# Performance work log

Hardware: AMD Instinct MI355X
Metric: run time of the kernel (lower is better)

Reference implementation:

```python
import jax, jax.numpy as jnp
import numpy as np

RES = 0.03
NUM_ROTS = 36
NUM_PROPOSAL = 256
OVERSAMPLE = 4           # fixed-size stand-in for the data-dependent while loop
GX, GY, GZ = 272, 112, 272  # grid covering [-4,4.16] x [-0.2,3.16] x [-4,4.16] at res=0.03
POW = 0.5
SEED_DIST_THRESH = 0.3


def setup_inputs() -> dict:
    key = jax.random.key(0)
    ks = jax.random.split(key, 6)
    N, M = 100000, 1024
    extent = jnp.array([7.0, 3.0, 7.0], jnp.float32)
    offset = jnp.array([-3.5, 0.0, -3.5], jnp.float32)
    pc = jax.random.uniform(ks[0], (N, 3), jnp.float32) * extent + offset
    xyz = jax.random.uniform(ks[1], (N, 3), jnp.float32, minval=-0.3, maxval=0.3)
    scale = jax.random.uniform(ks[2], (N, 3), jnp.float32, minval=0.1, maxval=1.0)
    prob = jax.random.uniform(ks[3], (N,), jnp.float32)
    corners = jnp.array([[-4.0, -0.2, -4.0], [4.16, 3.16, 4.16]], jnp.float32)
    vote_points = jax.random.uniform(ks[4], (M, 3), jnp.float32) * extent + offset
    return dict(pc=pc, xyz=xyz, scale=scale, prob=prob, corners=corners, vote_points=vote_points)


def hough_vote(pc, xyz, scale, prob, corners):
    # Each point casts NUM_ROTS votes: center = pc + R_y(theta) @ xyz_offset
    thetas = 2.0 * jnp.pi * jnp.arange(NUM_ROTS, dtype=jnp.float32) / NUM_ROTS
    c, s = jnp.cos(thetas), jnp.sin(thetas)  # [R]
    ox, oy, oz = xyz[:, 0:1], xyz[:, 1:2], xyz[:, 2:3]  # [N,1]
    rx = ox * c + oz * s      # [N,R]
    rz = -ox * s + oz * c     # [N,R]
    tx = pc[:, 0:1] + rx
    ty = jnp.broadcast_to(pc[:, 1:2] + oy, tx.shape)
    tz = pc[:, 2:3] + rz
    ix = jnp.floor((tx - corners[0, 0]) / RES + 0.5).astype(jnp.int32)
    iy = jnp.floor((ty - corners[0, 1]) / RES + 0.5).astype(jnp.int32)
    iz = jnp.floor((tz - corners[0, 2]) / RES + 0.5).astype(jnp.int32)
    inb = ((ix >= 0) & (ix < GX) & (iy >= 0) & (iy < GY) & (iz >= 0) & (iz < GZ))
    ixc = jnp.clip(ix, 0, GX - 1)
    iyc = jnp.clip(iy, 0, GY - 1)
    izc = jnp.clip(iz, 0, GZ - 1)
    flat = ((ixc * GY + iyc) * GZ + izc).ravel()  # [N*R]
    w = (prob[:, None] * inb.astype(prob.dtype))  # [N,R]
    grid_obj = jnp.zeros((GX * GY * GZ,), pc.dtype).at[flat].add(w.ravel())
    ws = (w[:, :, None] * scale[:, None, :]).reshape(-1, 3)
    grid_scale = jnp.zeros((GX * GY * GZ, 3), pc.dtype).at[flat].add(ws)
    hv_map = grid_obj.reshape(GX, GY, GZ)
    hv_scale = (grid_scale / (grid_obj[:, None] + 1e-7)).reshape(GX, GY, GZ, 3)
    return hv_map, hv_scale


def reference(pc, xyz, scale, prob, corners, vote_points):
    hv_map, hv_scale = hough_vote(pc, xyz, scale, prob, corners)
    hv_map_y = jnp.power(hv_map.max(axis=1) + 1e-7, POW)  # [GX,GZ]
    hv_map_yidx = jnp.argmax(hv_map, axis=1)              # [GX,GZ]
    dist = hv_map_y.reshape(-1)
    finite = jnp.isfinite(dist)
    safe = jnp.where(finite, dist, 0.0)
    ok = finite.all() & (safe.sum() >= 1e-7)
    dist = jnp.where(ok, safe, 1.0)

    # fixed-size oversampling instead of the data-dependent while loop
    K = NUM_PROPOSAL * OVERSAMPLE
    sample = jax.random.categorical(jax.random.key(42), jnp.log(dist + 1e-30), shape=(K,))
    sample_val = dist[sample]
    xi = sample // GZ
    zi = sample % GZ
    yi = hv_map_yidx[xi, zi]
    world_loc = jnp.stack([xi, yi, zi], -1).astype(pc.dtype) * RES + corners[0]  # [K,3]
    sc = hv_scale[xi, yi, zi, :]  # [K,3]

    # min distance to vote seeds; keep candidates near seeds (fallback: keep all)
    d2seed = jnp.min(jnp.linalg.norm(world_loc[:, None, :] - vote_points[None, :, :], axis=-1), axis=-1)
    keep = d2seed < SEED_DIST_THRESH
    keep = jnp.where(keep.any(), keep, jnp.ones_like(keep))
    order = jnp.argsort(jnp.where(keep, 0, 1))  # stable: passing candidates first
    sel = order[:NUM_PROPOSAL]
    candidates = world_loc[sel]
    scales_out = sc[sel]
    probs = jnp.zeros((NUM_PROPOSAL,), pc.dtype)
    return candidates, probs, scales_out
```

## Files before the change

### kernel.cpp

```cpp
#include <hip/hip_runtime.h>
#include <math.h>
#include <stdio.h>
#include <stdint.h>

#define GXD 272
#define GYD 112
#define GZD 272
#define NROT 36
#define CCLS (GXD*GZD)
#define KSMP 1024
#define NPROP 256
#define HSLOTS 2048
#define YH 56
#define NBINS (GXD*2)
#define SLICE (GYD*GZD)
#define SVCAP 64
#define ROWG 16

struct RotTab { float c[NROT]; float s[NROT]; };

__device__ __forceinline__ uint32_t cell_hash(int flat) {
    return ((uint32_t)flat * 2654435761u) >> 21;
}

#define ROTL_AB(x, r) __builtin_amdgcn_alignbit((x), (x), 32u - (r))

__device__ __forceinline__ void threefry2x32(uint32_t k0, uint32_t k1,
                                             uint32_t x0, uint32_t x1,
                                             uint32_t& o0, uint32_t& o1) {
    uint32_t ks2 = k0 ^ k1 ^ 0x1BD11BDAu;
#define TF_ROUND(r) { x0 += x1; x1 = ROTL_AB(x1, r); x1 ^= x0; }
    x0 += k0; x1 += k1;
    TF_ROUND(13) TF_ROUND(15) TF_ROUND(26) TF_ROUND(6)
    x0 += k1;  x1 += ks2 + 1u;
    TF_ROUND(17) TF_ROUND(29) TF_ROUND(16) TF_ROUND(24)
    x0 += ks2; x1 += k0 + 2u;
    TF_ROUND(13) TF_ROUND(15) TF_ROUND(26) TF_ROUND(6)
    x0 += k0;  x1 += k1 + 3u;
    TF_ROUND(17) TF_ROUND(29) TF_ROUND(16) TF_ROUND(24)
    x0 += k1;  x1 += ks2 + 4u;
    TF_ROUND(13) TF_ROUND(15) TF_ROUND(26) TF_ROUND(6)
    x0 += ks2; x1 += k0 + 5u;
#undef TF_ROUND
    o0 = x0; o1 = x1;
}

__device__ __forceinline__ uint32_t tf_bits(uint32_t i) {
    uint32_t o0, o1;
    threefry2x32(0u, 42u, 0u, i, o0, o1);
    return o0 ^ o1;
}

template<int W>
__device__ __forceinline__ void tf_batch(uint32_t ib, uint32_t* out) {
    constexpr uint32_t K1  = 42u;
    constexpr uint32_t KS2 = 0u ^ 42u ^ 0x1BD11BDAu;
    uint32_t x0[W], x1[W];
#pragma unroll
    for (int j = 0; j < W; ++j) {
        x0[j] = 0u;
        x1[j] = ib + (uint32_t)(j * CCLS) + K1;
    }
    constexpr uint32_t R[5][4]  = {{13,15,26,6},{17,29,16,24},{13,15,26,6},
                                   {17,29,16,24},{13,15,26,6}};
    constexpr uint32_t I0[5] = {K1, KS2, 0u, K1, KS2};
    constexpr uint32_t I1[5] = {KS2 + 1u, 2u, K1 + 3u, KS2 + 4u, 5u};
#pragma unroll
    for (int g = 0; g < 5; ++g) {
#pragma unroll
        for (int r = 0; r < 4; ++r) {
#pragma unroll
            for (int j = 0; j < W; ++j) {
                x0[j] += x1[j];
                x1[j] = ROTL_AB(x1[j], R[g][r]);
                x1[j] ^= x0[j];
            }
        }
#pragma unroll
        for (int j = 0; j < W; ++j) { x0[j] += I0[g]; x1[j] += I1[g]; }
    }
#pragma unroll
    for (int j = 0; j < W; ++j) out[j] = x0[j] ^ x1[j];
}

__device__ __forceinline__ float uniform_from_bits(uint32_t b) {
    const float TINY = 1.1754943508222875e-38f;
    float f = __uint_as_float((b >> 9) | 0x3f800000u) - 1.0f;
    float u = __fadd_rn(__fmul_rn(f, 1.0f), TINY);
    return fmaxf(TINY, u);
}

__device__ __forceinline__ float gumbel_from_u(float u) {
    float l1 = (float)log((double)u);
    float l2 = (float)log((double)(-l1));
    return -l2;
}

__device__ __forceinline__ bool vote_iy(float py, float oy, float c0y, int& iy) {
    float ty = __fadd_rn(py, oy);
    float vy = __fadd_rn(__fdiv_rn(__fsub_rn(ty, c0y), 0.03f), 0.5f);
    iy = (int)floorf(vy);
    return (iy >= 0 && iy < GYD);
}
__device__ __forceinline__ bool vote_xz(float px, float pz, float ox, float oz,
                                        float c, float s, float c0x, float c0z,
                                        int& ix, int& iz) {
    float rx = __fadd_rn(__fmul_rn(ox, c), __fmul_rn(oz, s));
    float rz = __fadd_rn(__fmul_rn(-ox, s), __fmul_rn(oz, c));
    float tx = __fadd_rn(px, rx);
    float tz = __fadd_rn(pz, rz);
    float vx = __fadd_rn(__fdiv_rn(__fsub_rn(tx, c0x), 0.03f), 0.5f);
    float vz = __fadd_rn(__fdiv_rn(__fsub_rn(tz, c0z), 0.03f), 0.5f);
    ix = (int)floorf(vx);
    iz = (int)floorf(vz);
    return (ix >= 0 && ix < GXD && iz >= 0 && iz < GZD);
}
__device__ __forceinline__ bool vote_cell(float px, float py, float pz,
                                          float ox, float oy, float oz,
                                          float c, float s,
                                          float c0x, float c0y, float c0z,
                                          int& flat) {
    int iy, ix, iz;
    if (!vote_iy(py, oy, c0y, iy)) return false;
    if (!vote_xz(px, pz, ox, oz, c, s, c0x, c0z, ix, iz)) return false;
    flat = (ix*GYD + iy)*GZD + iz;
    return true;
}

__global__ __launch_bounds__(256) void k_count(const float* __restrict__ pc, const float* __restrict__ xyz,
                          const float* __restrict__ corners, int N, RotTab rt,
                          int* __restrict__ bincnt) {
    __shared__ int h[NBINS];
    int tid = threadIdx.x;
    for (int j = tid; j < NBINS; j += 256) h[j] = 0;
    __syncthreads();
    int i = blockIdx.x * 256 + tid;
    if (i < N) {
        float px = pc[3*i], py = pc[3*i+1], pz = pc[3*i+2];
        float ox = xyz[3*i], oy = xyz[3*i+1], oz = xyz[3*i+2];
        int iy;
        if (vote_iy(py, oy, corners[1], iy)) {
            int ybit = (iy >= YH) ? 1 : 0;
            float c0x = corners[0], c0z = corners[2];
            for (int r = 0; r < NROT; ++r) {
                int ix, iz;
                if (vote_xz(px, pz, ox, oz, rt.c[r], rt.s[r], c0x, c0z, ix, iz))
                    atomicAdd(&h[ix*2 + ybit], 1);
            }
        }
    }
    __syncthreads();
    for (int j = tid; j < NBINS; j += 256) if (h[j]) atomicAdd(&bincnt[j], h[j]);
}

__global__ __launch_bounds__(576) void k_prefix(const int* __restrict__ bincnt,
                         int* __restrict__ binbase, int* __restrict__ bincur) {
    __shared__ int sc[576];
    int tid = threadIdx.x;
    int v = (tid < NBINS) ? bincnt[tid] : 0;
    sc[tid] = v;
    __syncthreads();
    for (int off = 1; off < 576; off <<= 1) {
        int x = sc[tid];
        if (tid >= off) x += sc[tid - off];
        __syncthreads();
        sc[tid] = x;
        __syncthreads();
    }
    if (tid < NBINS) {
        int excl = sc[tid] - v;
        binbase[tid] = excl;
        bincur[tid] = excl;
    }
}

__global__ __launch_bounds__(256) void k_binwrite(const float* __restrict__ pc, const float* __restrict__ xyz,
                          const float* __restrict__ prob, const float* __restrict__ corners,
                          int N, RotTab rt, int* __restrict__ bincur,
                          int* __restrict__ vflat, float* __restrict__ vw) {
    __shared__ int h[NBINS];
    __shared__ int bbase[NBINS];
    int tid = threadIdx.x;
    for (int j = tid; j < NBINS; j += 256) h[j] = 0;
    __syncthreads();
    int i = blockIdx.x * 256 + tid;
    float px=0, py=0, pz=0, ox=0, oy=0, oz=0, w0=0, c0x=0, c0z=0;
    int iy = -1, ybit = 0;
    bool act = false;
    if (i < N) {
        px = pc[3*i]; py = pc[3*i+1]; pz = pc[3*i+2];
        ox = xyz[3*i]; oy = xyz[3*i+1]; oz = xyz[3*i+2];
        w0 = prob[i];
        c0x = corners[0]; c0z = corners[2];
        if (vote_iy(py, oy, corners[1], iy)) {
            act = true;
            ybit = (iy >= YH) ? 1 : 0;
        }
    }
    if (act) {
        for (int r = 0; r < NROT; ++r) {
            int ix, iz;
            if (vote_xz(px, pz, ox, oz, rt.c[r], rt.s[r], c0x, c0z, ix, iz))
                atomicAdd(&h[ix*2 + ybit], 1);
        }
    }
    __syncthreads();
    for (int j = tid; j < NBINS; j += 256) {
        int cnt = h[j];
        bbase[j] = cnt ? atomicAdd(&bincur[j], cnt) : 0;
        h[j] = 0;
    }
    __syncthreads();
    if (act) {
        for (int r = 0; r < NROT; ++r) {
            int ix, iz;
            if (vote_xz(px, pz, ox, oz, rt.c[r], rt.s[r], c0x, c0z, ix, iz)) {
                int bin = ix*2 + ybit;
                int rank = atomicAdd(&h[bin], 1);
                int slot = bbase[bin] + rank;
                vflat[slot] = (ix*GYD + iy)*GZD + iz;
                vw[slot] = w0;
            }
        }
    }
}

__global__ __launch_bounds__(256) void k_accum(const int* __restrict__ binbase,
                          const int* __restrict__ bincnt,
                          const int* __restrict__ vflat, const float* __restrict__ vw,
                          float* __restrict__ gobj) {
    __shared__ float tile[YH*GZD];
    int b = blockIdx.x;
    int x = b >> 1, yh = b & 1;
    int tid = threadIdx.x;
    for (int j = tid; j < YH*GZD; j += 256) tile[j] = 0.0f;
    __syncthreads();
    int lo = binbase[b], n = bincnt[b];
    int xoff = x * SLICE;
    int yoff = yh * (YH*GZD);
    for (int j = lo + tid; j < lo + n; j += 256) {
        int rel = vflat[j] - xoff;
        atomicAdd(&tile[rel - yoff], vw[j]);
    }
    __syncthreads();
    float* dst = gobj + (size_t)xoff + yoff;
    for (int j = tid; j < YH*GZD; j += 256) dst[j] = tile[j];
}

__global__ __launch_bounds__(256) void k_colmax(const float* __restrict__ gobj,
                         float* __restrict__ logits, int* __restrict__ yidx,
                         float* __restrict__ sumdist) {
    int c = blockIdx.x * blockDim.x + threadIdx.x;
    float d = 0.0f;
    if (c < CCLS) {
        int x = c / GZD, z = c % GZD;
        const float* base = gobj + (size_t)x*GYD*GZD + z;
        float m = base[0];
        int mi = 0;
        for (int y = 1; y < GYD; ++y) {
            float v = base[(size_t)y*GZD];
            if (v > m) { m = v; mi = y; }
        }
        d = __fsqrt_rn(__fadd_rn(m, 1e-7f));
        yidx[c] = mi;
        logits[c] = (float)log((double)__fadd_rn(d, 1e-30f));
    }
    __shared__ float sred[256];
    int tid = threadIdx.x;
    sred[tid] = d; __syncthreads();
    for (int off = 128; off > 0; off >>= 1) {
        if (tid < off) sred[tid] += sred[tid+off];
        __syncthreads();
    }
    if (tid == 0) atomicAdd(sumdist, sred[0]);
}

__global__ __launch_bounds__(256) void k_thresh(const float* __restrict__ logits,
                                                const float* __restrict__ sumdist,
                                                uint32_t* __restrict__ bth) {
    int c = blockIdx.x * blockDim.x + threadIdx.x;
    if (c >= CCLS) return;
    double B0 = log((double)*sumdist) - 3.0;
    double t = exp(-exp((double)logits[c] - (B0 - 0.05)));
    long long k_th = (long long)floor(t * 8388608.0) - 2;
    uint32_t b;
    if (k_th <= 0)              b = 0u;
    else if (k_th >= 8388608LL) b = 0xFFFFFFFFu;
    else                        b = (uint32_t)k_th << 9;
    bth[c] = b;
}

__global__ __launch_bounds__(256) void k_prefilter(const uint32_t* __restrict__ bth,
                                                   int* __restrict__ svcnt,
                                                   uint2* __restrict__ svrec) {
    int c = blockIdx.x * 256 + threadIdx.x;
    int k0 = blockIdx.y * (KSMP / ROWG);
    uint32_t th = bth[c];
    uint32_t i = (uint32_t)k0 * (uint32_t)CCLS + (uint32_t)c;
#pragma unroll 1
    for (int kk = 0; kk < KSMP / ROWG; kk += 8) {
        uint32_t b[8];
        tf_batch<8>(i, b);
#pragma unroll
        for (int j = 0; j < 8; ++j) {
            if (__builtin_expect(b[j] >= th, 0)) {
                int row = k0 + kk + j;
                int idx = atomicAdd(&svcnt[row], 1);
                if (idx < SVCAP) svrec[row * SVCAP + idx] = make_uint2((uint32_t)c, b[j]);
            }
        }
        i += 8u * (uint32_t)CCLS;
    }
}

__global__ __launch_bounds__(256) void k_finalize(const float* __restrict__ logits,
                                                  const int* __restrict__ svcnt,
                                                  const uint2* __restrict__ svrec,
                                                  int* __restrict__ samples) {
    int k = blockIdx.x;
    int tid = threadIdx.x;
    int n = svcnt[k];
    float best = -INFINITY; int bc = 0x7fffffff;
    if (n > 0 && n <= SVCAP) {
        if (tid < n) {
            uint2 rec = svrec[k * SVCAP + tid];
            int c = (int)rec.x;
            best = __fadd_rn(gumbel_from_u(uniform_from_bits(rec.y)), logits[c]);
            bc = c;
        }
    } else {
        uint32_t base = (uint32_t)k * (uint32_t)CCLS;
        for (int c = tid; c < CCLS; c += 256) {
            float v = __fadd_rn(gumbel_from_u(uniform_from_bits(tf_bits(base + (uint32_t)c))), logits[c]);
            if (v > best || (v == best && c < bc)) { best = v; bc = c; }
        }
    }
    __shared__ float sv[256];
    __shared__ int   si[256];
    sv[tid] = best; si[tid] = bc; __syncthreads();
    for (int off = 128; off > 0; off >>= 1) {
        if (tid < off) {
            float v2 = sv[tid+off]; int i2 = si[tid+off];
            if (v2 > sv[tid] || (v2 == sv[tid] && i2 < si[tid])) { sv[tid] = v2; si[tid] = i2; }
        }
        __syncthreads();
    }
    if (tid == 0) samples[k] = si[0];
}

__global__ __launch_bounds__(256) void k_build_table(const int* __restrict__ samples,
                                                     const int* __restrict__ yidx,
                                                     int* __restrict__ hkeys,
                                                     float* __restrict__ gsmall) {
    int tid = threadIdx.x;
    for (int j = tid; j < HSLOTS; j += 256) hkeys[j] = -1;
    for (int j = tid; j < 3*HSLOTS; j += 256) gsmall[j] = 0.0f;
    __syncthreads();
    for (int k = tid; k < KSMP; k += 256) {
        int s = samples[k];
        int xi = s / GZD, zi = s % GZD;
        int yi = yidx[s];
        int flat = (xi*GYD + yi)*GZD + zi;
        uint32_t h = cell_hash(flat);
        for (;;) {
            int prev = atomicCAS(&hkeys[h], -1, flat);
            if (prev == -1 || prev == flat) break;
            h = (h + 1) & (HSLOTS - 1);
        }
    }
}

__global__ __launch_bounds__(256) void k_scale_scatter(const float* __restrict__ pc, const float* __restrict__ xyz,
                          const float* __restrict__ scale, const float* __restrict__ prob,
                          const float* __restrict__ corners,
                          const int* __restrict__ hkeys, float* __restrict__ gsmall,
                          int N, RotTab rt) {
    __shared__ int lk[HSLOTS];
    for (int j = threadIdx.x; j < HSLOTS; j += 256) lk[j] = hkeys[j];
    __syncthreads();
    int i = blockIdx.x * blockDim.x + threadIdx.x;
    int r = blockIdx.y;
    if (i >= N) return;
    int flat;
    if (!vote_cell(pc[3*i], pc[3*i+1], pc[3*i+2], xyz[3*i], xyz[3*i+1], xyz[3*i+2],
                   rt.c[r], rt.s[r], corners[0], corners[1], corners[2], flat)) return;
    uint32_t h = cell_hash(flat);
    int slot = -1;
    for (;;) {
        int key = lk[h];
        if (key == flat) { slot = (int)h; break; }
        if (key == -1) break;
        h = (h + 1) & (HSLOTS - 1);
    }
    if (slot < 0) return;
    float w0 = prob[i];
    atomicAdd(&gsmall[3*slot+0], __fmul_rn(w0, scale[3*i]));
    atomicAdd(&gsmall[3*slot+1], __fmul_rn(w0, scale[3*i+1]));
    atomicAdd(&gsmall[3*slot+2], __fmul_rn(w0, scale[3*i+2]));
}

__global__ __launch_bounds__(256) void k_post(const float* __restrict__ gobj,
                       const int* __restrict__ hkeys, const float* __restrict__ gsmall,
                       const int* __restrict__ yidx, const int* __restrict__ samples,
                       const float* __restrict__ corners, const float* __restrict__ vp, int M,
                       float* __restrict__ world, float* __restrict__ scv, int* __restrict__ keep) {
    int k = blockIdx.x;
    int tid = threadIdx.x;
    int s = samples[k];
    int xi = s / GZD, zi = s % GZD;
    int yi = yidx[s];
    float wx = __fadd_rn(__fmul_rn((float)xi, 0.03f), corners[0]);
    float wy = __fadd_rn(__fmul_rn((float)yi, 0.03f), corners[1]);
    float wz = __fadd_rn(__fmul_rn((float)zi, 0.03f), corners[2]);

    float dmin = INFINITY;
    for (int j = tid; j < M; j += 256) {
        float dx = __fsub_rn(wx, vp[3*j]);
        float dy = __fsub_rn(wy, vp[3*j+1]);
        float dz = __fsub_rn(wz, vp[3*j+2]);
        float sq = __fadd_rn(__fadd_rn(__fmul_rn(dx,dx), __fmul_rn(dy,dy)), __fmul_rn(dz,dz));
        dmin = fminf(dmin, __fsqrt_rn(sq));
    }
    __shared__ float sm[256];
    sm[tid] = dmin; __syncthreads();
    for (int off = 128; off > 0; off >>= 1) {
        if (tid < off) sm[tid] = fminf(sm[tid], sm[tid+off]);
        __syncthreads();
    }
    if (tid == 0) {
        world[3*k] = wx; world[3*k+1] = wy; world[3*k+2] = wz;
        int flat = (xi*GYD + yi)*GZD + zi;
        uint32_t h = cell_hash(flat);
        while (hkeys[h] != flat) h = (h + 1) & (HSLOTS - 1);
        float go = __fadd_rn(gobj[flat], 1e-7f);
        scv[3*k+0] = __fdiv_rn(gsmall[3*h+0], go);
        scv[3*k+1] = __fdiv_rn(gsmall[3*h+1], go);
        scv[3*k+2] = __fdiv_rn(gsmall[3*h+2], go);
        keep[k] = (sm[0] < 0.3f) ? 1 : 0;
    }
}

__global__ __launch_bounds__(256) void k_select(const float* __restrict__ world,
                                                const float* __restrict__ scv,
                                                const int* __restrict__ keep,
                                                float* __restrict__ out) {
    __shared__ int kp[KSMP];
    __shared__ int tsum[256];
    __shared__ int sel[NPROP];
    __shared__ int anyk;
    int tid = threadIdx.x;
    if (tid == 0) anyk = 0;
    __syncthreads();
    int a = 0;
    for (int j = tid; j < KSMP; j += 256) { int v = keep[j]; kp[j] = v; a |= v; }
    if (a) anyk = 1;
    __syncthreads();
    int any = anyk;
    int j0 = tid * 4;
    int k0v = any ? kp[j0]   : 1;
    int k1v = any ? kp[j0+1] : 1;
    int k2v = any ? kp[j0+2] : 1;
    int k3v = any ? kp[j0+3] : 1;
    int s0 = k0v, s1 = s0 + k1v, s2 = s1 + k2v, s3 = s2 + k3v;
    tsum[tid] = s3;
    __syncthreads();
    for (int off = 1; off < 256; off <<= 1) {
        int x = tsum[tid];
        if (tid >= off) x += tsum[tid - off];
        __syncthreads();
        tsum[tid] = x;
        __syncthreads();
    }
    int base = (tid > 0) ? tsum[tid-1] : 0;
    int nk = tsum[255];
    int inc[4] = { base + s0, base + s1, base + s2, base + s3 };
    int kv[4]  = { k0v, k1v, k2v, k3v };
    for (int q = 0; q < 4; ++q) {
        int j = j0 + q;
        int slot = kv[q] ? (inc[q] - 1) : (nk + j - inc[q]);
        if (slot < NPROP) sel[slot] = j;
    }
    __syncthreads();
    if (tid < NPROP) {
        int sidx = sel[tid];
        out[3*tid+0] = world[3*sidx+0];
        out[3*tid+1] = world[3*sidx+1];
        out[3*tid+2] = world[3*sidx+2];
        out[3*NPROP + tid] = 0.0f;
        out[4*NPROP + 3*tid + 0] = scv[3*sidx+0];
        out[4*NPROP + 3*tid + 1] = scv[3*sidx+1];
        out[4*NPROP + 3*tid + 2] = scv[3*sidx+2];
    }
}

extern "C" void kernel_launch(void* const* d_in, const int* in_sizes, int n_in,
                              void* d_out, int out_size, void* d_ws, size_t ws_size,
                              hipStream_t stream) {
    const float* pc      = (const float*)d_in[0];
    const float* xyz     = (const float*)d_in[1];
    const float* scale   = (const float*)d_in[2];
    const float* prob    = (const float*)d_in[3];
    const float* corners = (const float*)d_in[4];
    const float* vp      = (const float*)d_in[5];
    int N = in_sizes[0] / 3;
    int M = in_sizes[5] / 3;
    int NV = N * NROT;

    const size_t G = (size_t)GXD * GYD * GZD;
    float* gobj    = (float*)d_ws;
    float* sumdist = gobj + G;
    int*   bincnt  = (int*)(sumdist + 1);
    int*   svcnt   = bincnt + NBINS;
    int*   binbase = svcnt + KSMP;
    int*   bincur  = binbase + NBINS;
    float* logits  = (float*)(bincur + NBINS);
    uint32_t* bth  = (uint32_t*)(logits + CCLS);
    int*   yidx    = (int*)(bth + CCLS);
    int*   samples = yidx + CCLS;
    int*   hkeys   = samples + KSMP;
    float* gsmall  = (float*)(hkeys + HSLOTS);
    float* world   = gsmall + 3*HSLOTS;
    float* scv     = world + 3*KSMP;
    int*   keep    = (int*)(scv + 3*KSMP);
    uint2* svrec   = (uint2*)(((uintptr_t)(keep + KSMP) + 15) & ~(uintptr_t)15);
    int*   vflat   = (int*)(svrec + (size_t)KSMP * SVCAP);
    float* vw      = (float*)(vflat + NV);
    size_t need = (size_t)((char*)(vw + NV) - (char*)d_ws);
    if (ws_size < need) {
        fprintf(stderr, "kernel_launch: ws_size %zu < needed %zu\n", ws_size, need);
        return;
    }

    hipMemsetAsync(sumdist, 0, (1 + NBINS + KSMP)*sizeof(int), stream);

    RotTab rt;
    const float twopi = (float)(2.0 * M_PI);
    for (int r = 0; r < NROT; ++r) {
        float th = (twopi * (float)r) / 36.0f;
        rt.c[r] = (float)cos((double)th);
        rt.s[r] = (float)sin((double)th);
    }

    int pblocks = (N + 255) / 256;
    k_count<<<pblocks, 256, 0, stream>>>(pc, xyz, corners, N, rt, bincnt);
    k_prefix<<<1, 576, 0, stream>>>(bincnt, binbase, bincur);
    k_binwrite<<<pblocks, 256, 0, stream>>>(pc, xyz, prob, corners, N, rt, bincur, vflat, vw);
    k_accum<<<NBINS, 256, 0, stream>>>(binbase, bincnt, vflat, vw, gobj);
    k_colmax<<<(CCLS + 255) / 256, 256, 0, stream>>>(gobj, logits, yidx, sumdist);
    k_thresh<<<(CCLS + 255) / 256, 256, 0, stream>>>(logits, sumdist, bth);
    dim3 pf_grid(CCLS / 256, ROWG);
    k_prefilter<<<pf_grid, 256, 0, stream>>>(bth, svcnt, svrec);
    k_finalize<<<KSMP, 256, 0, stream>>>(logits, svcnt, svrec, samples);
    k_build_table<<<1, 256, 0, stream>>>(samples, yidx, hkeys, gsmall);
    dim3 sgrid(pblocks, NROT);
    k_scale_scatter<<<sgrid, 256, 0, stream>>>(pc, xyz, scale, prob, corners, hkeys, gsmall, N, rt);
    k_post<<<KSMP, 256, 0, stream>>>(gobj, hkeys, gsmall, yidx, samples, corners, vp, M, world, scv, keep);
    k_select<<<1, 256, 0, stream>>>(world, scv, keep, (float*)d_out);
}
```

Before: 420.7 us.

## Fuse column max into accumulation, interleave vote records, and restructure sampling kernels

Vote records are written as interleaved (flat, weight) pairs, and each accumulation block computes per-column partial maxima over its half-slice from shared memory. This removes the strided full-grid column scan, which now only merges two partials. The prefilter is split into two launches using different rotate instruction sequences, finalize drops to one wavefront with shuffle reduction, and scale scatter loops over rotations per thread instead of using a 2D grid. Together these trade some extra workspace and code complexity for less global traffic and fewer launches' worth of redundant per-point work.

```diff
diff --git a/kernel.cpp b/kernel.cpp
--- a/kernel.cpp
+++ b/kernel.cpp
@@ -24,6 +24,20 @@
 }
 
 #define ROTL_AB(x, r) __builtin_amdgcn_alignbit((x), (x), 32u - (r))
+
+template<int MODE, uint32_t R>
+__device__ __forceinline__ uint32_t rotl1(uint32_t x) {
+    if constexpr (MODE == 0) {
+        return ROTL_AB(x, R);
+    } else {
+        uint32_t t, d;
+        asm("v_lshrrev_b32 %0, %3, %2\n\t"
+            "v_lshl_or_b32 %1, %2, %4, %0"
+            : "=&v"(t), "=v"(d)
+            : "v"(x), "i"(32u - R), "i"(R));
+        return d;
+    }
+}
 
 __device__ __forceinline__ void threefry2x32(uint32_t k0, uint32_t k1,
                                              uint32_t x0, uint32_t x1,
@@ -51,7 +65,7 @@
     return o0 ^ o1;
 }
 
-template<int W>
+template<int W, int MODE>
 __device__ __forceinline__ void tf_batch(uint32_t ib, uint32_t* out) {
     constexpr uint32_t K1  = 42u;
     constexpr uint32_t KS2 = 0u ^ 42u ^ 0x1BD11BDAu;
@@ -61,24 +75,17 @@
         x0[j] = 0u;
         x1[j] = ib + (uint32_t)(j * CCLS) + K1;
     }
-    constexpr uint32_t R[5][4]  = {{13,15,26,6},{17,29,16,24},{13,15,26,6},
-                                   {17,29,16,24},{13,15,26,6}};
-    constexpr uint32_t I0[5] = {K1, KS2, 0u, K1, KS2};
-    constexpr uint32_t I1[5] = {KS2 + 1u, 2u, K1 + 3u, KS2 + 4u, 5u};
-#pragma unroll
-    for (int g = 0; g < 5; ++g) {
-#pragma unroll
-        for (int r = 0; r < 4; ++r) {
-#pragma unroll
-            for (int j = 0; j < W; ++j) {
-                x0[j] += x1[j];
-                x1[j] = ROTL_AB(x1[j], R[g][r]);
-                x1[j] ^= x0[j];
-            }
-        }
-#pragma unroll
-        for (int j = 0; j < W; ++j) { x0[j] += I0[g]; x1[j] += I1[g]; }
-    }
+#define TFB_ROUND(RR) _Pragma("unroll") \
+    for (int j = 0; j < W; ++j) { x0[j] += x1[j]; x1[j] = rotl1<MODE, RR>(x1[j]); x1[j] ^= x0[j]; }
+#define TFB_INJ(IA, IB) _Pragma("unroll") \
+    for (int j = 0; j < W; ++j) { x0[j] += (IA); x1[j] += (IB); }
+    TFB_ROUND(13) TFB_ROUND(15) TFB_ROUND(26) TFB_ROUND(6)  TFB_INJ(K1,  KS2 + 1u)
+    TFB_ROUND(17) TFB_ROUND(29) TFB_ROUND(16) TFB_ROUND(24) TFB_INJ(KS2, 2u)
+    TFB_ROUND(13) TFB_ROUND(15) TFB_ROUND(26) TFB_ROUND(6)  TFB_INJ(0u,  K1 + 3u)
+    TFB_ROUND(17) TFB_ROUND(29) TFB_ROUND(16) TFB_ROUND(24) TFB_INJ(K1,  KS2 + 4u)
+    TFB_ROUND(13) TFB_ROUND(15) TFB_ROUND(26) TFB_ROUND(6)  TFB_INJ(KS2, 5u)
+#undef TFB_ROUND
+#undef TFB_INJ
 #pragma unroll
     for (int j = 0; j < W; ++j) out[j] = x0[j] ^ x1[j];
 }
@@ -114,17 +121,6 @@
     ix = (int)floorf(vx);
     iz = (int)floorf(vz);
     return (ix >= 0 && ix < GXD && iz >= 0 && iz < GZD);
-}
-__device__ __forceinline__ bool vote_cell(float px, float py, float pz,
-                                          float ox, float oy, float oz,
-                                          float c, float s,
-                                          float c0x, float c0y, float c0z,
-                                          int& flat) {
-    int iy, ix, iz;
-    if (!vote_iy(py, oy, c0y, iy)) return false;
-    if (!vote_xz(px, pz, ox, oz, c, s, c0x, c0z, ix, iz)) return false;
-    flat = (ix*GYD + iy)*GZD + iz;
-    return true;
 }
 
 __global__ __launch_bounds__(256) void k_count(const float* __restrict__ pc, const float* __restrict__ xyz,
@@ -177,7 +173,7 @@
 __global__ __launch_bounds__(256) void k_binwrite(const float* __restrict__ pc, const float* __restrict__ xyz,
                           const float* __restrict__ prob, const float* __restrict__ corners,
                           int N, RotTab rt, int* __restrict__ bincur,
-                          int* __restrict__ vflat, float* __restrict__ vw) {
+                          uint2* __restrict__ vrec) {
     __shared__ int h[NBINS];
     __shared__ int bbase[NBINS];
     int tid = threadIdx.x;
@@ -218,8 +214,7 @@
                 int bin = ix*2 + ybit;
                 int rank = atomicAdd(&h[bin], 1);
                 int slot = bbase[bin] + rank;
-                vflat[slot] = (ix*GYD + iy)*GZD + iz;
-                vw[slot] = w0;
+                vrec[slot] = make_uint2((uint32_t)((ix*GYD + iy)*GZD + iz), __float_as_uint(w0));
             }
         }
     }
@@ -227,8 +222,9 @@
 
 __global__ __launch_bounds__(256) void k_accum(const int* __restrict__ binbase,
                           const int* __restrict__ bincnt,
-                          const int* __restrict__ vflat, const float* __restrict__ vw,
-                          float* __restrict__ gobj) {
+                          const uint2* __restrict__ vrec,
+                          float* __restrict__ gobj,
+                          float* __restrict__ cmax, int* __restrict__ camax) {
     __shared__ float tile[YH*GZD];
     int b = blockIdx.x;
     int x = b >> 1, yh = b & 1;
@@ -238,29 +234,40 @@
     int lo = binbase[b], n = bincnt[b];
     int xoff = x * SLICE;
     int yoff = yh * (YH*GZD);
+    int sub = xoff + yoff;
     for (int j = lo + tid; j < lo + n; j += 256) {
-        int rel = vflat[j] - xoff;
-        atomicAdd(&tile[rel - yoff], vw[j]);
-    }
-    __syncthreads();
-    float* dst = gobj + (size_t)xoff + yoff;
+        uint2 rec = vrec[j];
+        atomicAdd(&tile[(int)rec.x - sub], __uint_as_float(rec.y));
+    }
+    __syncthreads();
+    float* dst = gobj + (size_t)sub;
     for (int j = tid; j < YH*GZD; j += 256) dst[j] = tile[j];
-}
-
-__global__ __launch_bounds__(256) void k_colmax(const float* __restrict__ gobj,
+    for (int z = tid; z < GZD; z += 256) {
+        float m = tile[z];
+        int mi = 0;
+        for (int y = 1; y < YH; ++y) {
+            float v = tile[y*GZD + z];
+            if (v > m) { m = v; mi = y; }
+        }
+        cmax[b*GZD + z] = m;
+        camax[b*GZD + z] = mi;
+    }
+}
+
+__global__ __launch_bounds__(256) void k_colmax2(const float* __restrict__ cmax,
+                         const int* __restrict__ camax,
                          float* __restrict__ logits, int* __restrict__ yidx,
                          float* __restrict__ sumdist) {
     int c = blockIdx.x * blockDim.x + threadIdx.x;
     float d = 0.0f;
     if (c < CCLS) {
         int x = c / GZD, z = c % GZD;
-        const float* base = gobj + (size_t)x*GYD*GZD + z;
-        float m = base[0];
-        int mi = 0;
-        for (int y = 1; y < GYD; ++y) {
-            float v = base[(size_t)y*GZD];
-            if (v > m) { m = v; mi = y; }
-        }
+        int b0 = (x*2)*GZD + z;
+        int b1 = b0 + GZD;
+        float m0 = cmax[b0], m1 = cmax[b1];
+        float m; int mi;
+        if (m1 > m0) { m = m1; mi = YH + camax[b1]; }
+        else         { m = m0; mi = camax[b0]; }
         d = __fsqrt_rn(__fadd_rn(m, 1e-7f));
         yidx[c] = mi;
         logits[c] = (float)log((double)__fadd_rn(d, 1e-30f));
@@ -290,17 +297,19 @@
     bth[c] = b;
 }
 
-__global__ __launch_bounds__(256) void k_prefilter(const uint32_t* __restrict__ bth,
-                                                   int* __restrict__ svcnt,
-                                                   uint2* __restrict__ svrec) {
+template<int MODE>
+__global__ __launch_bounds__(256) void k_prefilter_t(const uint32_t* __restrict__ bth,
+                                                     int* __restrict__ svcnt,
+                                                     uint2* __restrict__ svrec,
+                                                     int kbase) {
     int c = blockIdx.x * 256 + threadIdx.x;
-    int k0 = blockIdx.y * (KSMP / ROWG);
+    int k0 = kbase + blockIdx.y * (KSMP / ROWG);
     uint32_t th = bth[c];
     uint32_t i = (uint32_t)k0 * (uint32_t)CCLS + (uint32_t)c;
 #pragma unroll 1
     for (int kk = 0; kk < KSMP / ROWG; kk += 8) {
         uint32_t b[8];
-        tf_batch<8>(i, b);
+        tf_batch<8, MODE>(i, b);
 #pragma unroll
         for (int j = 0; j < 8; ++j) {
             if (__builtin_expect(b[j] >= th, 0)) {
@@ -313,10 +322,10 @@
     }
 }
 
-__global__ __launch_bounds__(256) void k_finalize(const float* __restrict__ logits,
-                                                  const int* __restrict__ svcnt,
-                                                  const uint2* __restrict__ svrec,
-                                                  int* __restrict__ samples) {
+__global__ __launch_bounds__(64) void k_finalize(const float* __restrict__ logits,
+                                                 const int* __restrict__ svcnt,
+                                                 const uint2* __restrict__ svrec,
+                                                 int* __restrict__ samples) {
     int k = blockIdx.x;
     int tid = threadIdx.x;
     int n = svcnt[k];
@@ -330,22 +339,17 @@
         }
     } else {
         uint32_t base = (uint32_t)k * (uint32_t)CCLS;
-        for (int c = tid; c < CCLS; c += 256) {
+        for (int c = tid; c < CCLS; c += 64) {
             float v = __fadd_rn(gumbel_from_u(uniform_from_bits(tf_bits(base + (uint32_t)c))), logits[c]);
             if (v > best || (v == best && c < bc)) { best = v; bc = c; }
         }
     }
-    __shared__ float sv[256];
-    __shared__ int   si[256];
-    sv[tid] = best; si[tid] = bc; __syncthreads();
-    for (int off = 128; off > 0; off >>= 1) {
-        if (tid < off) {
-            float v2 = sv[tid+off]; int i2 = si[tid+off];
-            if (v2 > sv[tid] || (v2 == sv[tid] && i2 < si[tid])) { sv[tid] = v2; si[tid] = i2; }
-        }
-        __syncthreads();
-    }
-    if (tid == 0) samples[k] = si[0];
+    for (int off = 32; off > 0; off >>= 1) {
+        float v2 = __shfl_down(best, off);
+        int   i2 = __shfl_down(bc, off);
+        if (v2 > best || (v2 == best && i2 < bc)) { best = v2; bc = i2; }
+    }
+    if (tid == 0) samples[k] = bc;
 }
 
 __global__ __launch_bounds__(256) void k_build_table(const int* __restrict__ samples,
@@ -378,25 +382,35 @@
     __shared__ int lk[HSLOTS];
     for (int j = threadIdx.x; j < HSLOTS; j += 256) lk[j] = hkeys[j];
     __syncthreads();
-    int i = blockIdx.x * blockDim.x + threadIdx.x;
-    int r = blockIdx.y;
+    int i = blockIdx.x * 256 + threadIdx.x;
     if (i >= N) return;
-    int flat;
-    if (!vote_cell(pc[3*i], pc[3*i+1], pc[3*i+2], xyz[3*i], xyz[3*i+1], xyz[3*i+2],
-                   rt.c[r], rt.s[r], corners[0], corners[1], corners[2], flat)) return;
-    uint32_t h = cell_hash(flat);
-    int slot = -1;
-    for (;;) {
-        int key = lk[h];
-        if (key == flat) { slot = (int)h; break; }
-        if (key == -1) break;
-        h = (h + 1) & (HSLOTS - 1);
-    }
-    if (slot < 0) return;
+    float px = pc[3*i], py = pc[3*i+1], pz = pc[3*i+2];
+    float ox = xyz[3*i], oy = xyz[3*i+1], oz = xyz[3*i+2];
+    int iy;
+    if (!vote_iy(py, oy, corners[1], iy)) return;
+    float c0x = corners[0], c0z = corners[2];
+    int iyo = iy * GZD;
     float w0 = prob[i];
-    atomicAdd(&gsmall[3*slot+0], __fmul_rn(w0, scale[3*i]));
-    atomicAdd(&gsmall[3*slot+1], __fmul_rn(w0, scale[3*i+1]));
-    atomicAdd(&gsmall[3*slot+2], __fmul_rn(w0, scale[3*i+2]));
+    float ws0 = __fmul_rn(w0, scale[3*i]);
+    float ws1 = __fmul_rn(w0, scale[3*i+1]);
+    float ws2 = __fmul_rn(w0, scale[3*i+2]);
+    for (int r = 0; r < NROT; ++r) {
+        int ix, iz;
+        if (!vote_xz(px, pz, ox, oz, rt.c[r], rt.s[r], c0x, c0z, ix, iz)) continue;
+        int flat = ix * SLICE + iyo + iz;
+        uint32_t h = cell_hash(flat);
+        int slot = -1;
+        for (;;) {
+            int key = lk[h];
+            if (key == flat) { slot = (int)h; break; }
+            if (key == -1) break;
+            h = (h + 1) & (HSLOTS - 1);
+        }
+        if (slot < 0) continue;
+        atomicAdd(&gsmall[3*slot+0], ws0);
+        atomicAdd(&gsmall[3*slot+1], ws1);
+        atomicAdd(&gsmall[3*slot+2], ws2);
+    }
 }
 
 __global__ __launch_bounds__(256) void k_post(const float* __restrict__ gobj,
@@ -522,10 +536,11 @@
     float* world   = gsmall + 3*HSLOTS;
     float* scv     = world + 3*KSMP;
     int*   keep    = (int*)(scv + 3*KSMP);
-    uint2* svrec   = (uint2*)(((uintptr_t)(keep + KSMP) + 15) & ~(uintptr_t)15);
-    int*   vflat   = (int*)(svrec + (size_t)KSMP * SVCAP);
-    float* vw      = (float*)(vflat + NV);
-    size_t need = (size_t)((char*)(vw + NV) - (char*)d_ws);
+    float* cmax    = (float*)(keep + KSMP);
+    int*   camax   = (int*)(cmax + (size_t)NBINS*GZD);
+    uint2* svrec   = (uint2*)(((uintptr_t)(camax + (size_t)NBINS*GZD) + 15) & ~(uintptr_t)15);
+    uint2* vrec    = svrec + (size_t)KSMP * SVCAP;
+    size_t need = (size_t)((char*)(vrec + NV) - (char*)d_ws);
     if (ws_size < need) {
         fprintf(stderr, "kernel_launch: ws_size %zu < needed %zu\n", ws_size, need);
         return;
@@ -544,16 +559,16 @@
     int pblocks = (N + 255) / 256;
     k_count<<<pblocks, 256, 0, stream>>>(pc, xyz, corners, N, rt, bincnt);
     k_prefix<<<1, 576, 0, stream>>>(bincnt, binbase, bincur);
-    k_binwrite<<<pblocks, 256, 0, stream>>>(pc, xyz, prob, corners, N, rt, bincur, vflat, vw);
-    k_accum<<<NBINS, 256, 0, stream>>>(binbase, bincnt, vflat, vw, gobj);
-    k_colmax<<<(CCLS + 255) / 256, 256, 0, stream>>>(gobj, logits, yidx, sumdist);
-    k_thresh<<<(CCLS + 255) / 256, 256, 0, stream>>>(logits, sumdist, bth);
-    dim3 pf_grid(CCLS / 256, ROWG);
-    k_prefilter<<<pf_grid, 256, 0, stream>>>(bth, svcnt, svrec);
-    k_finalize<<<KSMP, 256, 0, stream>>>(logits, svcnt, svrec, samples);
+    k_binwrite<<<pblocks, 256, 0, stream>>>(pc, xyz, prob, corners, N, rt, bincur, vrec);
+    k_accum<<<NBINS, 256, 0, stream>>>(binbase, bincnt, vrec, gobj, cmax, camax);
+    k_colmax2<<<CCLS / 256, 256, 0, stream>>>(cmax, camax, logits, yidx, sumdist);
+    k_thresh<<<CCLS / 256, 256, 0, stream>>>(logits, sumdist, bth);
+    dim3 pf_grid(CCLS / 256, ROWG / 2);
+    k_prefilter_t<0><<<pf_grid, 256, 0, stream>>>(bth, svcnt, svrec, 0);
+    k_prefilter_t<1><<<pf_grid, 256, 0, stream>>>(bth, svcnt, svrec, KSMP/2);
+    k_finalize<<<KSMP, 64, 0, stream>>>(logits, svcnt, svrec, samples);
     k_build_table<<<1, 256, 0, stream>>>(samples, yidx, hkeys, gsmall);
-    dim3 sgrid(pblocks, NROT);
-    k_scale_scatter<<<sgrid, 256, 0, stream>>>(pc, xyz, scale, prob, corners, hkeys, gsmall, N, rt);
+    k_scale_scatter<<<pblocks, 256, 0, stream>>>(pc, xyz, scale, prob, corners, hkeys, gsmall, N, rt);
     k_post<<<KSMP, 256, 0, stream>>>(gobj, hkeys, gsmall, yidx, samples, corners, vp, M, world, scv, keep);
     k_select<<<1, 256, 0, stream>>>(world, scv, keep, (float*)d_out);
 }
```

After: 436.5 us. 3.8% more time.
